# Performance work log

Measured on AMD Instinct MI355X. Metric: run time of the kernel, lower is better.

The kernel has to match this reference:

```python
import jax, jax.numpy as jnp
import numpy as np
import math

N_NODES = 50000
N_EDGES = 800000
D_NODE = 128
D_EDGE = 64  # 4 + dist_embed_dim(60)
N_HEADS = 8
HEAD_DIM = D_NODE // N_HEADS


def setup_inputs() -> dict:
    key = jax.random.key(0)
    ks = jax.random.split(key, 8)
    scale_q = 1.0 / math.sqrt(D_NODE)
    scale_kv = 1.0 / math.sqrt(D_NODE + D_EDGE)
    return {
        "node_feats": jax.random.normal(ks[0], (N_NODES, D_NODE), jnp.float32),
        "edge_feats": jax.random.normal(ks[1], (N_EDGES, D_EDGE), jnp.float32),
        "edge_index": jax.random.randint(ks[2], (2, N_EDGES), 0, N_NODES, jnp.int32),
        "Wq": jax.random.normal(ks[3], (D_NODE, D_NODE), jnp.float32) * scale_q,
        "bq": jnp.zeros((D_NODE,), jnp.float32),
        "Wk": jax.random.normal(ks[4], (D_NODE + D_EDGE, D_NODE), jnp.float32) * scale_kv,
        "bk": jnp.zeros((D_NODE,), jnp.float32),
        "Wv": jax.random.normal(ks[5], (D_NODE + D_EDGE, D_NODE), jnp.float32) * scale_kv,
        "bv": jnp.zeros((D_NODE,), jnp.float32),
        "Wo": jax.random.normal(ks[6], (D_NODE, D_NODE), jnp.float32) * scale_q,
        "bo": jnp.zeros((D_NODE,), jnp.float32),
    }


def reference(node_feats, edge_feats, edge_index, Wq, bq, Wk, bk, Wv, bv, Wo, bo):
    src, tgt = edge_index[0], edge_index[1]
    n = node_feats.shape[0]
    e = edge_feats.shape[0]

    # per-edge Q from target node, K/V from [source node || edge feats]
    q = (node_feats[tgt] @ Wq + bq).reshape(e, N_HEADS, HEAD_DIM)
    kv_input = jnp.concatenate([node_feats[src], edge_feats], axis=-1)  # [E, D_NODE+D_EDGE]
    k = (kv_input @ Wk + bk).reshape(e, N_HEADS, HEAD_DIM)
    v = (kv_input @ Wv + bv).reshape(e, N_HEADS, HEAD_DIM)

    # per-edge attention logits [E, H]
    a = jnp.einsum("ehc,ehc->eh", q, k) / math.sqrt(HEAD_DIM)

    # segment softmax over edges grouped by target node (numerically stable)
    seg_max = jax.ops.segment_max(a, tgt, num_segments=n)      # [N, H]
    a = jnp.exp(a - seg_max[tgt])
    seg_sum = jax.ops.segment_sum(a, tgt, num_segments=n)      # [N, H]
    a = a / seg_sum[tgt]

    # weighted scatter-sum aggregate
    o = jax.ops.segment_sum(a[..., None] * v, tgt, num_segments=n)  # [N, H, C]
    out = o.reshape(n, N_HEADS * HEAD_DIM) @ Wo + bo
    return out  # dropout is identity at inference
```

## Files before the change

kernel.cpp:

```cpp
#include <hip/hip_runtime.h>

#define NND 50000
#define NED 800000
#define DN 128
#define DE 64
#define DKV 192
#define NH 8
#define HD 16

__device__ __forceinline__ float sane(float x) {
    return (x == x && fabsf(x) < 1e30f) ? x : 0.f;
}

__global__ __launch_bounds__(256) void node_proj_qkv(
    const float* __restrict__ nf,
    const float* __restrict__ Wq, const float* __restrict__ bq,
    const float* __restrict__ Wk, const float* __restrict__ bk,
    const float* __restrict__ Wv, const float* __restrict__ bv,
    float* __restrict__ Qn, float* __restrict__ Kn, float* __restrict__ Vn)
{
    __shared__ alignas(16) float xs[128][8];
    const int t = threadIdx.x;
    const int nb = blockIdx.x * 8;
    {
        const int node = t >> 5;
        const int k0 = (t & 31) * 4;
        const float4 x4 = *(const float4*)(nf + (size_t)(nb + node) * DN + k0);
        xs[k0 + 0][node] = x4.x;
        xs[k0 + 1][node] = x4.y;
        xs[k0 + 2][node] = x4.z;
        xs[k0 + 3][node] = x4.w;
    }
    __syncthreads();

    const int col = t & 127;
    const int grp = t >> 7;
    float aq[4], ak[4], av[4];
    const float bqv = bq[col], bkv = bk[col], bvv = bv[col];
#pragma unroll
    for (int i = 0; i < 4; i++) { aq[i] = bqv; ak[i] = bkv; av[i] = bvv; }

#pragma unroll 4
    for (int k = 0; k < 128; k++) {
        const float wq = Wq[k * DN + col];
        const float wk = Wk[k * DN + col];
        const float wv = Wv[k * DN + col];
        const float4 x = *(const float4*)&xs[k][grp * 4];
        aq[0] += x.x * wq; aq[1] += x.y * wq; aq[2] += x.z * wq; aq[3] += x.w * wq;
        ak[0] += x.x * wk; ak[1] += x.y * wk; ak[2] += x.z * wk; ak[3] += x.w * wk;
        av[0] += x.x * wv; av[1] += x.y * wv; av[2] += x.z * wv; av[3] += x.w * wv;
    }
#pragma unroll
    for (int i = 0; i < 4; i++) {
        const size_t r = (size_t)(nb + grp * 4 + i) * DN + col;
        Qn[r] = aq[i]; Kn[r] = ak[i]; Vn[r] = av[i];
    }
}

__global__ __launch_bounds__(256) void node_proj_q(
    const float* __restrict__ nf,
    const float* __restrict__ Wq, const float* __restrict__ bq,
    float* __restrict__ Qn)
{
    __shared__ alignas(16) float xs[128][8];
    const int t = threadIdx.x;
    const int nb = blockIdx.x * 8;
    {
        const int node = t >> 5;
        const int k0 = (t & 31) * 4;
        const float4 x4 = *(const float4*)(nf + (size_t)(nb + node) * DN + k0);
        xs[k0 + 0][node] = x4.x;
        xs[k0 + 1][node] = x4.y;
        xs[k0 + 2][node] = x4.z;
        xs[k0 + 3][node] = x4.w;
    }
    __syncthreads();

    const int col = t & 127;
    const int grp = t >> 7;
    float aq[4];
    const float bqv = bq[col];
#pragma unroll
    for (int i = 0; i < 4; i++) aq[i] = bqv;

#pragma unroll 4
    for (int k = 0; k < 128; k++) {
        const float wq = Wq[k * DN + col];
        const float4 x = *(const float4*)&xs[k][grp * 4];
        aq[0] += x.x * wq; aq[1] += x.y * wq; aq[2] += x.z * wq; aq[3] += x.w * wq;
    }
#pragma unroll
    for (int i = 0; i < 4; i++)
        Qn[(size_t)(nb + grp * 4 + i) * DN + col] = aq[i];
}

__global__ __launch_bounds__(256) void edge_hist(
    const int* __restrict__ eidx, int* __restrict__ cnt)
{
    const int e = blockIdx.x * 256 + threadIdx.x;
    atomicAdd(&cnt[eidx[NED + e]], 1);
}

#define SCAN_NB ((NND + 255) / 256)

__global__ __launch_bounds__(256) void scanA(
    const int* __restrict__ cnt, int* __restrict__ partial)
{
    const int idx = blockIdx.x * 256 + threadIdx.x;
    int v = (idx < NND) ? cnt[idx] : 0;
#pragma unroll
    for (int off = 1; off < 64; off <<= 1) v += __shfl_xor(v, off);
    __shared__ int wsum[4];
    if ((threadIdx.x & 63) == 0) wsum[threadIdx.x >> 6] = v;
    __syncthreads();
    if (threadIdx.x == 0)
        partial[blockIdx.x] = wsum[0] + wsum[1] + wsum[2] + wsum[3];
}

__global__ __launch_bounds__(256) void scanB(int* __restrict__ partial)
{
    __shared__ int s[256];
    const int t = threadIdx.x;
    const int v = (t < SCAN_NB) ? partial[t] : 0;
    s[t] = v;
    __syncthreads();
    for (int off = 1; off < 256; off <<= 1) {
        const int u = (t >= off) ? s[t - off] : 0;
        __syncthreads();
        s[t] += u;
        __syncthreads();
    }
    if (t < SCAN_NB) partial[t] = s[t] - v;
}

__global__ __launch_bounds__(256) void scanC(
    const int* __restrict__ cnt, const int* __restrict__ partial,
    int* __restrict__ offs)
{
    __shared__ int s[256];
    const int t = threadIdx.x;
    const int idx = blockIdx.x * 256 + t;
    const int v = (idx < NND) ? cnt[idx] : 0;
    s[t] = v;
    __syncthreads();
    for (int off = 1; off < 256; off <<= 1) {
        const int u = (t >= off) ? s[t - off] : 0;
        __syncthreads();
        s[t] += u;
        __syncthreads();
    }
    if (idx < NND) offs[idx] = partial[blockIdx.x] + s[t] - v;
}

__global__ __launch_bounds__(256) void edge_scatter(
    const int* __restrict__ eidx, int* __restrict__ offs, int2* __restrict__ epack)
{
    const int e = blockIdx.x * 256 + threadIdx.x;
    const int pos = atomicAdd(&offs[eidx[NED + e]], 1);
    epack[pos] = make_int2(e, eidx[e]);
}

__global__ __launch_bounds__(256) void edge_aggregate(
    const float* __restrict__ ef,
    const int* __restrict__ cnt, const int* __restrict__ offs,
    const int2* __restrict__ epack,
    const float* __restrict__ Wk, const float* __restrict__ Wv,
    const float* __restrict__ Kn, const float* __restrict__ Vn,
    float* qo)
{
    __shared__ alignas(16) float efs[4][8][64];
    const int t = threadIdx.x;
    const int w = t >> 6;
    const int l = t & 63;
    const int j = l & 7;
    const int es = l >> 3;
    const int node = blockIdx.x * 4 + w;

    const int end = offs[node];
    const int beg = end - cnt[node];

    const float* __restrict__ WkB = Wk + 128 * DN;
    const float* __restrict__ WvB = Wv + 128 * DN;

    const float2 q2 = *(const float2*)(qo + (size_t)node * DN + 2 * l);

    float qh[16];
#pragma unroll
    for (int m = 0; m < 8; m++) {
        qh[2 * m]     = __shfl(q2.x, (l & 56) + m);
        qh[2 * m + 1] = __shfl(q2.y, (l & 56) + m);
    }
    float qt[8];
#pragma unroll
    for (int i = 0; i < 8; i++) {
        const float* wrow = WkB + (j * 8 + i) * DN + (l & 56) * 2;
        const float4 w0 = *(const float4*)(wrow);
        const float4 w1 = *(const float4*)(wrow + 4);
        const float4 w2 = *(const float4*)(wrow + 8);
        const float4 w3 = *(const float4*)(wrow + 12);
        qt[i] = qh[0]  * w0.x + qh[1]  * w0.y + qh[2]  * w0.z + qh[3]  * w0.w
              + qh[4]  * w1.x + qh[5]  * w1.y + qh[6]  * w1.z + qh[7]  * w1.w
              + qh[8]  * w2.x + qh[9]  * w2.y + qh[10] * w2.z + qh[11] * w2.w
              + qh[12] * w3.x + qh[13] * w3.y + qh[14] * w3.z + qh[15] * w3.w;
    }

    float acc0 = 0.f, acc1 = 0.f, segacc = 0.f;
    float gt[8];
#pragma unroll
    for (int i = 0; i < 8; i++) gt[i] = 0.f;

    if (beg < end) {
        int2 ep = epack[min(beg + es, end - 1)];
        float4 A = *(const float4*)(ef + (size_t)ep.x * DE + j * 8);
        float4 B = *(const float4*)(ef + (size_t)ep.x * DE + j * 8 + 4);

        for (int base = beg; base < end; base += 8) {
            const int nbase = base + 8;
            int2 ep_n; float4 An, Bn;
            if (nbase < end) {
                ep_n = epack[min(nbase + es, end - 1)];
                An = *(const float4*)(ef + (size_t)ep_n.x * DE + j * 8);
                Bn = *(const float4*)(ef + (size_t)ep_n.x * DE + j * 8 + 4);
            }
            *(float4*)&efs[w][es][j * 8]     = A;
            *(float4*)&efs[w][es][j * 8 + 4] = B;

            float2 kn[8], vn[8];
#pragma unroll
            for (int e = 0; e < 8; e++) {
                const int se = __builtin_amdgcn_readlane(ep.y, e * 8);
                kn[e] = *(const float2*)(Kn + (size_t)se * DN + 2 * l);
                vn[e] = *(const float2*)(Vn + (size_t)se * DN + 2 * l);
            }

#pragma unroll
            for (int e = 0; e < 8; e++) {
                const float4 efA = *(const float4*)&efs[w][e][j * 8];
                const float4 efB = *(const float4*)&efs[w][e][j * 8 + 4];
                float part = q2.x * kn[e].x + q2.y * kn[e].y
                           + efA.x * qt[0] + efA.y * qt[1] + efA.z * qt[2] + efA.w * qt[3]
                           + efB.x * qt[4] + efB.y * qt[5] + efB.z * qt[6] + efB.w * qt[7];
                part += __shfl_xor(part, 1);
                part += __shfl_xor(part, 2);
                part += __shfl_xor(part, 4);
                const float arg = fminf(fmaxf(part * 0.25f, -60.f), 60.f);
                const float p = (base + e < end) ? __expf(arg) : 0.f;
                acc0 += p * vn[e].x;
                acc1 += p * vn[e].y;
                segacc += p;
                gt[0] += p * efA.x; gt[1] += p * efA.y; gt[2] += p * efA.z; gt[3] += p * efA.w;
                gt[4] += p * efB.x; gt[5] += p * efB.y; gt[6] += p * efB.z; gt[7] += p * efB.w;
            }
            ep = ep_n; A = An; B = Bn;
        }
    }

    float oe0 = 0.f, oe1 = 0.f;
#pragma unroll 16
    for (int k = 0; k < 64; k++) {
        const float g = __shfl(gt[k & 7], (l & 56) | (k >> 3));
        const float2 wv2 = *(const float2*)(WvB + k * DN + 2 * l);
        oe0 += g * wv2.x;
        oe1 += g * wv2.y;
    }
    acc0 += oe0;
    acc1 += oe1;

    const float r = (segacc > 0.f) ? 1.f / segacc : 0.f;
    float* orow = qo + (size_t)node * DN + 2 * l;
    orow[0] = sane(acc0 * r);
    orow[1] = sane(acc1 * r);
}

__global__ __launch_bounds__(256) void edge_pass_full(
    const float* __restrict__ nf, const float* __restrict__ ef,
    const int* __restrict__ eidx,
    const float* __restrict__ Wk, const float* __restrict__ bk,
    const float* __restrict__ Wv, const float* __restrict__ bv,
    const float* __restrict__ Qn,
    float* __restrict__ o_un, float* __restrict__ seg)
{
    __shared__ alignas(16) float kvs[4][192][4];
    const int t = threadIdx.x;
    const int w = t >> 6;
    const int l = t & 63;
    const int eb = blockIdx.x * 16 + w * 4;

    int src[4], tgt[4];
#pragma unroll
    for (int e = 0; e < 4; e++) {
        src[e] = eidx[eb + e];
        tgt[e] = eidx[NED + eb + e];
    }

#pragma unroll
    for (int it = 0; it < 3; it++) {
        const int idx = it * 64 + l;
        const int e = idx / 48;
        const int pos = (idx % 48) * 4;
        const float* p = (pos < 128)
            ? nf + (size_t)src[e] * DN + pos
            : ef + (size_t)(eb + e) * DE + (pos - 128);
        const float4 x4 = *(const float4*)p;
        kvs[w][pos + 0][e] = x4.x;
        kvs[w][pos + 1][e] = x4.y;
        kvs[w][pos + 2][e] = x4.z;
        kvs[w][pos + 3][e] = x4.w;
    }
    __syncthreads();

    const float bk0 = bk[2 * l], bk1 = bk[2 * l + 1];
    const float bv0 = bv[2 * l], bv1 = bv[2 * l + 1];
    float accK[4][2] = {{bk0,bk1},{bk0,bk1},{bk0,bk1},{bk0,bk1}};
    float accV[4][2] = {{bv0,bv1},{bv0,bv1},{bv0,bv1},{bv0,bv1}};

#pragma unroll 4
    for (int k = 0; k < DKV; k++) {
        const float4 e4 = *(const float4*)&kvs[w][k][0];
        const float2 wk2 = *(const float2*)(Wk + k * DN + 2 * l);
        const float2 wv2 = *(const float2*)(Wv + k * DN + 2 * l);
        accK[0][0] += e4.x * wk2.x; accK[0][1] += e4.x * wk2.y;
        accK[1][0] += e4.y * wk2.x; accK[1][1] += e4.y * wk2.y;
        accK[2][0] += e4.z * wk2.x; accK[2][1] += e4.z * wk2.y;
        accK[3][0] += e4.w * wk2.x; accK[3][1] += e4.w * wk2.y;
        accV[0][0] += e4.x * wv2.x; accV[0][1] += e4.x * wv2.y;
        accV[1][0] += e4.y * wv2.x; accV[1][1] += e4.y * wv2.y;
        accV[2][0] += e4.z * wv2.x; accV[2][1] += e4.z * wv2.y;
        accV[3][0] += e4.w * wv2.x; accV[3][1] += e4.w * wv2.y;
    }

    const int h = l >> 3;
#pragma unroll
    for (int e = 0; e < 4; e++) {
        const float2 q2 = *(const float2*)(Qn + (size_t)tgt[e] * DN + 2 * l);
        float part = q2.x * accK[e][0] + q2.y * accK[e][1];
        part += __shfl_xor(part, 1);
        part += __shfl_xor(part, 2);
        part += __shfl_xor(part, 4);
        float arg = fminf(fmaxf(part * 0.25f, -60.f), 60.f);
        const float p = __expf(arg);

        atomicAdd(&o_un[(size_t)tgt[e] * DN + 2 * l],     p * accV[e][0]);
        atomicAdd(&o_un[(size_t)tgt[e] * DN + 2 * l + 1], p * accV[e][1]);
        if ((l & 7) == 0) atomicAdd(&seg[tgt[e] * NH + h], p);
    }
}

__global__ __launch_bounds__(256) void out_proj(
    const float* o_un, const float* __restrict__ seg,
    const float* __restrict__ Wo, const float* __restrict__ bo,
    float* out)
{
    __shared__ alignas(16) float xs[128][8];
    const int t = threadIdx.x;
    const int nb = blockIdx.x * 8;
    {
        const int node = t >> 5;
        const int k0 = (t & 31) * 4;
        const float4 v = *(const float4*)(o_un + (size_t)(nb + node) * DN + k0);
        float r = 1.f;
        if (seg) {
            const float s = seg[(nb + node) * NH + (k0 >> 4)];
            r = (s > 0.f) ? 1.f / s : 0.f;
        }
        xs[k0 + 0][node] = sane(v.x * r);
        xs[k0 + 1][node] = sane(v.y * r);
        xs[k0 + 2][node] = sane(v.z * r);
        xs[k0 + 3][node] = sane(v.w * r);
    }
    __syncthreads();

    const int col = t & 127;
    const int grp = t >> 7;
    float acc[4];
    const float b = bo[col];
#pragma unroll
    for (int i = 0; i < 4; i++) acc[i] = b;

#pragma unroll 4
    for (int k = 0; k < 128; k++) {
        const float wo = Wo[k * DN + col];
        const float4 x = *(const float4*)&xs[k][grp * 4];
        acc[0] += x.x * wo; acc[1] += x.y * wo; acc[2] += x.z * wo; acc[3] += x.w * wo;
    }
#pragma unroll
    for (int i = 0; i < 4; i++)
        out[(size_t)(nb + grp * 4 + i) * DN + col] = acc[i];
}

extern "C" void kernel_launch(void* const* d_in, const int* in_sizes, int n_in,
                              void* d_out, int out_size, void* d_ws, size_t ws_size,
                              hipStream_t stream) {
    const float* nf   = (const float*)d_in[0];
    const float* ef   = (const float*)d_in[1];
    const int*   eidx = (const int*)d_in[2];
    const float* Wq   = (const float*)d_in[3];
    const float* bq   = (const float*)d_in[4];
    const float* Wk   = (const float*)d_in[5];
    const float* bk   = (const float*)d_in[6];
    const float* Wv   = (const float*)d_in[7];
    const float* bv   = (const float*)d_in[8];
    const float* Wo   = (const float*)d_in[9];
    const float* bo   = (const float*)d_in[10];
    float* out = (float*)d_out;

    float* Qn = out;

    const size_t tabBytes = (size_t)NND * DN * sizeof(float);
    const size_t csrBytes = 2 * tabBytes
                          + ((size_t)2 * NND + 2 * NED + SCAN_NB) * sizeof(int);
    const size_t accBytes = tabBytes + (size_t)NND * NH * sizeof(float);

    if (ws_size >= csrBytes) {
        float* Kn     = (float*)d_ws;
        float* Vn     = Kn + (size_t)NND * DN;
        int*   cnt    = (int*)(Vn + (size_t)NND * DN);
        int*   offs   = cnt + NND;
        int2*  epack  = (int2*)(offs + NND);
        int*   partial= (int*)(epack + NED);
        hipMemsetAsync(cnt, 0, NND * sizeof(int), stream);
        node_proj_qkv<<<NND / 8, 256, 0, stream>>>(nf, Wq, bq, Wk, bk, Wv, bv, Qn, Kn, Vn);
        edge_hist<<<NED / 256, 256, 0, stream>>>(eidx, cnt);
        scanA<<<SCAN_NB, 256, 0, stream>>>(cnt, partial);
        scanB<<<1, 256, 0, stream>>>(partial);
        scanC<<<SCAN_NB, 256, 0, stream>>>(cnt, partial, offs);
        edge_scatter<<<NED / 256, 256, 0, stream>>>(eidx, offs, epack);
        edge_aggregate<<<NND / 4, 256, 0, stream>>>(ef, cnt, offs, epack,
                                                    Wk, Wv, Kn, Vn, Qn);
        out_proj<<<NND / 8, 256, 0, stream>>>(Qn, nullptr, Wo, bo, out);
    } else {
        float* o_un = (float*)d_ws;
        float* seg  = o_un + (size_t)NND * DN;
        hipMemsetAsync(o_un, 0, accBytes, stream);
        node_proj_q<<<NND / 8, 256, 0, stream>>>(nf, Wq, bq, Qn);
        edge_pass_full<<<NED / 16, 256, 0, stream>>>(nf, ef, eidx, Wk, bk, Wv, bv, Qn, o_un, seg);
        out_proj<<<NND / 8, 256, 0, stream>>>(o_un, seg, Wo, bo, out);
    }
}
```

Measured before the change: 865.9 us.

## Retile node/out projections to 16 nodes per block and simplify edge aggregation loop

The QKV and output projections now process 16 nodes per block, 8 per thread, with a row-major shared tile and a 4-wide k step, so each weight load is reused across more nodes. The edge aggregation drops its software prefetch of the next 8 edges and loads K/V per edge inside the loop. It computes the q·Wk-edge term with a shuffle-reduction loop over 64 rows instead of broadcasting q. Nontemporal loads are used for node and edge features and the edge pack. These changes trade register pressure and lost prefetch overlap for better weight reuse and simpler code.

```diff
diff --git a/kernel.cpp b/kernel.cpp
--- a/kernel.cpp
+++ b/kernel.cpp
@@ -8,8 +8,20 @@
 #define NH 8
 #define HD 16
 
+typedef float f32x4 __attribute__((ext_vector_type(4)));
+typedef int   i32x2 __attribute__((ext_vector_type(2)));
+
 __device__ __forceinline__ float sane(float x) {
     return (x == x && fabsf(x) < 1e30f) ? x : 0.f;
+}
+
+__device__ __forceinline__ float4 nt_load4(const float* p) {
+    f32x4 v = __builtin_nontemporal_load((const f32x4*)p);
+    return make_float4(v.x, v.y, v.z, v.w);
+}
+__device__ __forceinline__ int2 nt_load2i(const int2* p) {
+    i32x2 v = __builtin_nontemporal_load((const i32x2*)p);
+    return make_int2(v.x, v.y);
 }
 
 __global__ __launch_bounds__(256) void node_proj_qkv(
@@ -18,6 +30,63 @@
     const float* __restrict__ Wk, const float* __restrict__ bk,
     const float* __restrict__ Wv, const float* __restrict__ bv,
     float* __restrict__ Qn, float* __restrict__ Kn, float* __restrict__ Vn)
+{
+    __shared__ alignas(16) float xs[16][128];
+    const int t = threadIdx.x;
+    const int nb = blockIdx.x * 16;
+#pragma unroll
+    for (int s = 0; s < 2; s++) {
+        const int idx = s * 256 + t;
+        const int node = idx >> 5;
+        const int k0 = (idx & 31) * 4;
+        const float4 x4 = nt_load4(nf + (size_t)(nb + node) * DN + k0);
+        *(float4*)&xs[node][k0] = x4;
+    }
+    __syncthreads();
+
+    const int col = t & 127;
+    const int g8 = (t >> 7) * 8;
+    float aq[8], ak[8], av[8];
+    const float bqv = bq[col], bkv = bk[col], bvv = bv[col];
+#pragma unroll
+    for (int n = 0; n < 8; n++) { aq[n] = bqv; ak[n] = bkv; av[n] = bvv; }
+
+#pragma unroll 2
+    for (int kk = 0; kk < 128; kk += 4) {
+        float4 xv[8];
+#pragma unroll
+        for (int n = 0; n < 8; n++) xv[n] = *(const float4*)&xs[g8 + n][kk];
+
+        const float wq0 = Wq[(kk + 0) * DN + col];
+        const float wq1 = Wq[(kk + 1) * DN + col];
+        const float wq2 = Wq[(kk + 2) * DN + col];
+        const float wq3 = Wq[(kk + 3) * DN + col];
+        const float wk0 = Wk[(kk + 0) * DN + col];
+        const float wk1 = Wk[(kk + 1) * DN + col];
+        const float wk2 = Wk[(kk + 2) * DN + col];
+        const float wk3 = Wk[(kk + 3) * DN + col];
+        const float wv0 = Wv[(kk + 0) * DN + col];
+        const float wv1 = Wv[(kk + 1) * DN + col];
+        const float wv2 = Wv[(kk + 2) * DN + col];
+        const float wv3 = Wv[(kk + 3) * DN + col];
+#pragma unroll
+        for (int n = 0; n < 8; n++) {
+            aq[n] += xv[n].x * wq0 + xv[n].y * wq1 + xv[n].z * wq2 + xv[n].w * wq3;
+            ak[n] += xv[n].x * wk0 + xv[n].y * wk1 + xv[n].z * wk2 + xv[n].w * wk3;
+            av[n] += xv[n].x * wv0 + xv[n].y * wv1 + xv[n].z * wv2 + xv[n].w * wv3;
+        }
+    }
+#pragma unroll
+    for (int n = 0; n < 8; n++) {
+        const size_t r = (size_t)(nb + g8 + n) * DN + col;
+        Qn[r] = aq[n]; Kn[r] = ak[n]; Vn[r] = av[n];
+    }
+}
+
+__global__ __launch_bounds__(256) void node_proj_q(
+    const float* __restrict__ nf,
+    const float* __restrict__ Wq, const float* __restrict__ bq,
+    float* __restrict__ Qn)
 {
     __shared__ alignas(16) float xs[128][8];
     const int t = threadIdx.x;
@@ -35,49 +104,6 @@
 
     const int col = t & 127;
     const int grp = t >> 7;
-    float aq[4], ak[4], av[4];
-    const float bqv = bq[col], bkv = bk[col], bvv = bv[col];
-#pragma unroll
-    for (int i = 0; i < 4; i++) { aq[i] = bqv; ak[i] = bkv; av[i] = bvv; }
-
-#pragma unroll 4
-    for (int k = 0; k < 128; k++) {
-        const float wq = Wq[k * DN + col];
-        const float wk = Wk[k * DN + col];
-        const float wv = Wv[k * DN + col];
-        const float4 x = *(const float4*)&xs[k][grp * 4];
-        aq[0] += x.x * wq; aq[1] += x.y * wq; aq[2] += x.z * wq; aq[3] += x.w * wq;
-        ak[0] += x.x * wk; ak[1] += x.y * wk; ak[2] += x.z * wk; ak[3] += x.w * wk;
-        av[0] += x.x * wv; av[1] += x.y * wv; av[2] += x.z * wv; av[3] += x.w * wv;
-    }
-#pragma unroll
-    for (int i = 0; i < 4; i++) {
-        const size_t r = (size_t)(nb + grp * 4 + i) * DN + col;
-        Qn[r] = aq[i]; Kn[r] = ak[i]; Vn[r] = av[i];
-    }
-}
-
-__global__ __launch_bounds__(256) void node_proj_q(
-    const float* __restrict__ nf,
-    const float* __restrict__ Wq, const float* __restrict__ bq,
-    float* __restrict__ Qn)
-{
-    __shared__ alignas(16) float xs[128][8];
-    const int t = threadIdx.x;
-    const int nb = blockIdx.x * 8;
-    {
-        const int node = t >> 5;
-        const int k0 = (t & 31) * 4;
-        const float4 x4 = *(const float4*)(nf + (size_t)(nb + node) * DN + k0);
-        xs[k0 + 0][node] = x4.x;
-        xs[k0 + 1][node] = x4.y;
-        xs[k0 + 2][node] = x4.z;
-        xs[k0 + 3][node] = x4.w;
-    }
-    __syncthreads();
-
-    const int col = t & 127;
-    const int grp = t >> 7;
     float aq[4];
     const float bqv = bq[col];
 #pragma unroll
@@ -173,7 +199,6 @@
     const int w = t >> 6;
     const int l = t & 63;
     const int j = l & 7;
-    const int es = l >> 3;
     const int node = blockIdx.x * 4 + w;
 
     const int end = offs[node];
@@ -184,24 +209,17 @@
 
     const float2 q2 = *(const float2*)(qo + (size_t)node * DN + 2 * l);
 
-    float qh[16];
-#pragma unroll
-    for (int m = 0; m < 8; m++) {
-        qh[2 * m]     = __shfl(q2.x, (l & 56) + m);
-        qh[2 * m + 1] = __shfl(q2.y, (l & 56) + m);
-    }
     float qt[8];
 #pragma unroll
-    for (int i = 0; i < 8; i++) {
-        const float* wrow = WkB + (j * 8 + i) * DN + (l & 56) * 2;
-        const float4 w0 = *(const float4*)(wrow);
-        const float4 w1 = *(const float4*)(wrow + 4);
-        const float4 w2 = *(const float4*)(wrow + 8);
-        const float4 w3 = *(const float4*)(wrow + 12);
-        qt[i] = qh[0]  * w0.x + qh[1]  * w0.y + qh[2]  * w0.z + qh[3]  * w0.w
-              + qh[4]  * w1.x + qh[5]  * w1.y + qh[6]  * w1.z + qh[7]  * w1.w
-              + qh[8]  * w2.x + qh[9]  * w2.y + qh[10] * w2.z + qh[11] * w2.w
-              + qh[12] * w3.x + qh[13] * w3.y + qh[14] * w3.z + qh[15] * w3.w;
+    for (int i = 0; i < 8; i++) qt[i] = 0.f;
+#pragma unroll 16
+    for (int k = 0; k < 64; k++) {
+        const float2 wk2 = *(const float2*)(WkB + k * DN + 2 * l);
+        float part = q2.x * wk2.x + q2.y * wk2.y;
+        part += __shfl_xor(part, 1);
+        part += __shfl_xor(part, 2);
+        part += __shfl_xor(part, 4);
+        if (j == (k >> 3)) qt[k & 7] = part;
     }
 
     float acc0 = 0.f, acc1 = 0.f, segacc = 0.f;
@@ -209,49 +227,34 @@
 #pragma unroll
     for (int i = 0; i < 8; i++) gt[i] = 0.f;
 
-    if (beg < end) {
-        int2 ep = epack[min(beg + es, end - 1)];
-        float4 A = *(const float4*)(ef + (size_t)ep.x * DE + j * 8);
-        float4 B = *(const float4*)(ef + (size_t)ep.x * DE + j * 8 + 4);
-
-        for (int base = beg; base < end; base += 8) {
-            const int nbase = base + 8;
-            int2 ep_n; float4 An, Bn;
-            if (nbase < end) {
-                ep_n = epack[min(nbase + es, end - 1)];
-                An = *(const float4*)(ef + (size_t)ep_n.x * DE + j * 8);
-                Bn = *(const float4*)(ef + (size_t)ep_n.x * DE + j * 8 + 4);
-            }
-            *(float4*)&efs[w][es][j * 8]     = A;
-            *(float4*)&efs[w][es][j * 8 + 4] = B;
-
-            float2 kn[8], vn[8];
-#pragma unroll
-            for (int e = 0; e < 8; e++) {
-                const int se = __builtin_amdgcn_readlane(ep.y, e * 8);
-                kn[e] = *(const float2*)(Kn + (size_t)se * DN + 2 * l);
-                vn[e] = *(const float2*)(Vn + (size_t)se * DN + 2 * l);
-            }
-
-#pragma unroll
-            for (int e = 0; e < 8; e++) {
-                const float4 efA = *(const float4*)&efs[w][e][j * 8];
-                const float4 efB = *(const float4*)&efs[w][e][j * 8 + 4];
-                float part = q2.x * kn[e].x + q2.y * kn[e].y
-                           + efA.x * qt[0] + efA.y * qt[1] + efA.z * qt[2] + efA.w * qt[3]
-                           + efB.x * qt[4] + efB.y * qt[5] + efB.z * qt[6] + efB.w * qt[7];
-                part += __shfl_xor(part, 1);
-                part += __shfl_xor(part, 2);
-                part += __shfl_xor(part, 4);
-                const float arg = fminf(fmaxf(part * 0.25f, -60.f), 60.f);
-                const float p = (base + e < end) ? __expf(arg) : 0.f;
-                acc0 += p * vn[e].x;
-                acc1 += p * vn[e].y;
-                segacc += p;
-                gt[0] += p * efA.x; gt[1] += p * efA.y; gt[2] += p * efA.z; gt[3] += p * efA.w;
-                gt[4] += p * efB.x; gt[5] += p * efB.y; gt[6] += p * efB.z; gt[7] += p * efB.w;
-            }
-            ep = ep_n; A = An; B = Bn;
+    for (int base = beg; base < end; base += 8) {
+        const int myE = min(base + (l >> 3), end - 1);
+        const int2 ep = nt_load2i(&epack[myE]);
+        const float4 A = nt_load4(ef + (size_t)ep.x * DE + j * 8);
+        const float4 B = nt_load4(ef + (size_t)ep.x * DE + j * 8 + 4);
+        *(float4*)&efs[w][l >> 3][j * 8]     = A;
+        *(float4*)&efs[w][l >> 3][j * 8 + 4] = B;
+
+#pragma unroll
+        for (int e = 0; e < 8; e++) {
+            const int se = __builtin_amdgcn_readlane(ep.y, e * 8);
+            const float4 efA = *(const float4*)&efs[w][e][j * 8];
+            const float4 efB = *(const float4*)&efs[w][e][j * 8 + 4];
+            const float2 kn2 = *(const float2*)(Kn + (size_t)se * DN + 2 * l);
+            float part = q2.x * kn2.x + q2.y * kn2.y
+                       + efA.x * qt[0] + efA.y * qt[1] + efA.z * qt[2] + efA.w * qt[3]
+                       + efB.x * qt[4] + efB.y * qt[5] + efB.z * qt[6] + efB.w * qt[7];
+            part += __shfl_xor(part, 1);
+            part += __shfl_xor(part, 2);
+            part += __shfl_xor(part, 4);
+            const float arg = fminf(fmaxf(part * 0.25f, -60.f), 60.f);
+            const float p = (base + e < end) ? __expf(arg) : 0.f;
+            const float2 vn2 = *(const float2*)(Vn + (size_t)se * DN + 2 * l);
+            acc0 += p * vn2.x;
+            acc1 += p * vn2.y;
+            segacc += p;
+            gt[0] += p * efA.x; gt[1] += p * efA.y; gt[2] += p * efA.z; gt[3] += p * efA.w;
+            gt[4] += p * efB.x; gt[5] += p * efB.y; gt[6] += p * efB.z; gt[7] += p * efB.w;
         }
     }
 
@@ -351,41 +354,52 @@
     const float* __restrict__ Wo, const float* __restrict__ bo,
     float* out)
 {
-    __shared__ alignas(16) float xs[128][8];
-    const int t = threadIdx.x;
-    const int nb = blockIdx.x * 8;
-    {
-        const int node = t >> 5;
-        const int k0 = (t & 31) * 4;
+    __shared__ alignas(16) float xs[16][128];
+    const int t = threadIdx.x;
+    const int nb = blockIdx.x * 16;
+#pragma unroll
+    for (int s = 0; s < 2; s++) {
+        const int idx = s * 256 + t;
+        const int node = idx >> 5;
+        const int k0 = (idx & 31) * 4;
         const float4 v = *(const float4*)(o_un + (size_t)(nb + node) * DN + k0);
         float r = 1.f;
         if (seg) {
-            const float s = seg[(nb + node) * NH + (k0 >> 4)];
-            r = (s > 0.f) ? 1.f / s : 0.f;
+            const float sv = seg[(nb + node) * NH + (k0 >> 4)];
+            r = (sv > 0.f) ? 1.f / sv : 0.f;
         }
-        xs[k0 + 0][node] = sane(v.x * r);
-        xs[k0 + 1][node] = sane(v.y * r);
-        xs[k0 + 2][node] = sane(v.z * r);
-        xs[k0 + 3][node] = sane(v.w * r);
+        float4 o4;
+        o4.x = sane(v.x * r);
+        o4.y = sane(v.y * r);
+        o4.z = sane(v.z * r);
+        o4.w = sane(v.w * r);
+        *(float4*)&xs[node][k0] = o4;
     }
     __syncthreads();
 
     const int col = t & 127;
-    const int grp = t >> 7;
-    float acc[4];
+    const int g8 = (t >> 7) * 8;
+    float acc[8];
     const float b = bo[col];
 #pragma unroll
-    for (int i = 0; i < 4; i++) acc[i] = b;
-
-#pragma unroll 4
-    for (int k = 0; k < 128; k++) {
-        const float wo = Wo[k * DN + col];
-        const float4 x = *(const float4*)&xs[k][grp * 4];
-        acc[0] += x.x * wo; acc[1] += x.y * wo; acc[2] += x.z * wo; acc[3] += x.w * wo;
-    }
-#pragma unroll
-    for (int i = 0; i < 4; i++)
-        out[(size_t)(nb + grp * 4 + i) * DN + col] = acc[i];
+    for (int n = 0; n < 8; n++) acc[n] = b;
+
+#pragma unroll 2
+    for (int kk = 0; kk < 128; kk += 4) {
+        float4 xv[8];
+#pragma unroll
+        for (int n = 0; n < 8; n++) xv[n] = *(const float4*)&xs[g8 + n][kk];
+        const float w0 = Wo[(kk + 0) * DN + col];
+        const float w1 = Wo[(kk + 1) * DN + col];
+        const float w2 = Wo[(kk + 2) * DN + col];
+        const float w3 = Wo[(kk + 3) * DN + col];
+#pragma unroll
+        for (int n = 0; n < 8; n++)
+            acc[n] += xv[n].x * w0 + xv[n].y * w1 + xv[n].z * w2 + xv[n].w * w3;
+    }
+#pragma unroll
+    for (int n = 0; n < 8; n++)
+        out[(size_t)(nb + g8 + n) * DN + col] = acc[n];
 }
 
 extern "C" void kernel_launch(void* const* d_in, const int* in_sizes, int n_in,
@@ -418,8 +432,8 @@
         int*   offs   = cnt + NND;
         int2*  epack  = (int2*)(offs + NND);
         int*   partial= (int*)(epack + NED);
-        hipMemsetAsync(cnt, 0, NND * sizeof(int), stream);
-        node_proj_qkv<<<NND / 8, 256, 0, stream>>>(nf, Wq, bq, Wk, bk, Wv, bv, Qn, Kn, Vn);
+        (void)hipMemsetAsync(cnt, 0, NND * sizeof(int), stream);
+        node_proj_qkv<<<NND / 16, 256, 0, stream>>>(nf, Wq, bq, Wk, bk, Wv, bv, Qn, Kn, Vn);
         edge_hist<<<NED / 256, 256, 0, stream>>>(eidx, cnt);
         scanA<<<SCAN_NB, 256, 0, stream>>>(cnt, partial);
         scanB<<<1, 256, 0, stream>>>(partial);
@@ -427,13 +441,13 @@
         edge_scatter<<<NED / 256, 256, 0, stream>>>(eidx, offs, epack);
         edge_aggregate<<<NND / 4, 256, 0, stream>>>(ef, cnt, offs, epack,
                                                     Wk, Wv, Kn, Vn, Qn);
-        out_proj<<<NND / 8, 256, 0, stream>>>(Qn, nullptr, Wo, bo, out);
+        out_proj<<<NND / 16, 256, 0, stream>>>(Qn, nullptr, Wo, bo, out);
     } else {
         float* o_un = (float*)d_ws;
         float* seg  = o_un + (size_t)NND * DN;
-        hipMemsetAsync(o_un, 0, accBytes, stream);
+        (void)hipMemsetAsync(o_un, 0, accBytes, stream);
         node_proj_q<<<NND / 8, 256, 0, stream>>>(nf, Wq, bq, Qn);
         edge_pass_full<<<NED / 16, 256, 0, stream>>>(nf, ef, eidx, Wk, bk, Wv, bv, Qn, o_un, seg);
-        out_proj<<<NND / 8, 256, 0, stream>>>(o_un, seg, Wo, bo, out);
-    }
-}
+        out_proj<<<NND / 16, 256, 0, stream>>>(o_un, seg, Wo, bo, out);
+    }
+}
```

New measurement: 789.7 us. 8.8% less time.
